# Optimization experiments

Measured on AMD Instinct MI355X. Metric: run time of the kernel, lower is better.

## Reference

```python
import jax, jax.numpy as jnp
import numpy as np

H = 32      # query heads
KV = 8      # kv heads
D = 128     # head_dim
HID = 4096
S = 4       # num sequences
L = 1024    # tokens per sequence
N = S * L   # total tokens
EPS = 1e-6
THETA = 10000.0
GROUPS = H // KV


def setup_inputs() -> dict:
    key = jax.random.key(0)
    ks = jax.random.split(key, 12)
    def w(k, shape, std):
        return jax.random.normal(k, shape, dtype=jnp.float32) * std
    return {
        "hidden": w(ks[0], (N, HID), 1.0),
        "mu_prev": w(ks[1], (N, HID), 1.0),
        "positions": jnp.tile(jnp.arange(L, dtype=jnp.int32), S),
        "Wq": w(ks[2], (H * D, HID), HID ** -0.5),
        "Wk": w(ks[3], (KV * D, HID), HID ** -0.5),
        "Wv": w(ks[4], (KV * D, HID), HID ** -0.5),
        "Wo": w(ks[5], (HID, H * D), (H * D) ** -0.5),
        "Wmq": w(ks[6], (H * D, HID), 0.01),
        "Wmk": w(ks[7], (KV * D, HID), 0.01),
        "Wmv": w(ks[8], (KV * D, HID), 0.01),
        "q_norm_w": jnp.ones((D,), jnp.float32),
        "k_norm_w": jnp.ones((D,), jnp.float32),
    }


def _rmsnorm(x, w):
    var = jnp.mean(jnp.square(x), axis=-1, keepdims=True)
    return x * jax.lax.rsqrt(var + EPS) * w


def _rope_cos_sin(positions):
    inv_freq = 1.0 / (THETA ** (jnp.arange(0, D, 2, dtype=jnp.float32) / D))  # [D/2]
    freqs = positions.astype(jnp.float32)[:, None] * inv_freq[None, :]        # [N, D/2]
    emb = jnp.concatenate([freqs, freqs], axis=-1)                            # [N, D]
    return jnp.cos(emb), jnp.sin(emb)


def _rotate_half(x):
    x1, x2 = jnp.split(x, 2, axis=-1)
    return jnp.concatenate([-x2, x1], axis=-1)


def _apply_rotary(x, cos, sin):
    # x: [N, h, D]; cos/sin: [N, D]
    return x * cos[:, None, :] + _rotate_half(x) * sin[:, None, :]


def reference(hidden, mu_prev, positions, Wq, Wk, Wv, Wo, Wmq, Wmk, Wmv, q_norm_w, k_norm_w):
    # QKV projections + mu-bias fusion
    q = hidden @ Wq.T + mu_prev @ Wmq.T     # [N, H*D]
    k = hidden @ Wk.T + mu_prev @ Wmk.T     # [N, KV*D]
    v = hidden @ Wv.T + mu_prev @ Wmv.T     # [N, KV*D]
    q = q.reshape(N, H, D)
    k = k.reshape(N, KV, D)
    v = v.reshape(N, KV, D)
    # QK RMSNorm
    q = _rmsnorm(q, q_norm_w)
    k = _rmsnorm(k, k_norm_w)
    # RoPE
    cos, sin = _rope_cos_sin(positions)
    q = _apply_rotary(q, cos, sin)
    k = _apply_rotary(k, cos, sin)
    # GQA: expand kv heads to match q heads
    k = jnp.repeat(k, GROUPS, axis=1)       # [N, H, D]
    v = jnp.repeat(v, GROUPS, axis=1)
    # Varlen causal attention: equal-length seqs -> batched [S, L, H, D]
    qs = q.reshape(S, L, H, D)
    ks = k.reshape(S, L, H, D)
    vs = v.reshape(S, L, H, D)
    scale = 1.0 / np.sqrt(D)
    scores = jnp.einsum("slhd,smhd->shlm", qs, ks) * scale   # [S, H, L, L]
    causal = jnp.tril(jnp.ones((L, L), dtype=bool))
    scores = jnp.where(causal, scores, jnp.finfo(scores.dtype).min)
    probs = jax.nn.softmax(scores, axis=-1)
    out = jnp.einsum("shlm,smhd->slhd", probs, vs)           # [S, L, H, D]
    out = out.reshape(N, H * D)
    return out @ Wo.T                                         # [N, HID]
```

## Files before the change

### kernel.cpp

```cpp
#include <hip/hip_runtime.h>
#include <hip/hip_bf16.h>
#include <stdint.h>

#define DEV static __device__ __forceinline__

typedef __bf16 bf16_t;
typedef __bf16 bf16x8 __attribute__((ext_vector_type(8)));
typedef __bf16 bf16x4 __attribute__((ext_vector_type(4)));
typedef float  f32x4  __attribute__((ext_vector_type(4)));


DEV void gload_lds16(const void* g, void* l) {
  __builtin_amdgcn_global_load_lds(
      (__attribute__((address_space(1))) void*)(uintptr_t)(g),
      (__attribute__((address_space(3))) void*)(uintptr_t)(l),
      16, 0, 0);
}

#define BARRIER() asm volatile("s_barrier" ::: "memory")
#define MFMA16(a, b, c) __builtin_amdgcn_mfma_f32_16x16x32_bf16((a), (b), (c), 0, 0, 0)

DEV void pack_pair_chunk(const float* __restrict__ A, const float* __restrict__ B,
                         bf16_t* __restrict__ dst, size_t i) {
  size_t r = i >> 10, c = i & 1023;
  float4 va = ((const float4*)A)[i];
  float4 vb = ((const float4*)B)[i];
  bf16x4 oa = {(bf16_t)va.x, (bf16_t)va.y, (bf16_t)va.z, (bf16_t)va.w};
  bf16x4 ob = {(bf16_t)vb.x, (bf16_t)vb.y, (bf16_t)vb.z, (bf16_t)vb.w};
  ((bf16x4*)dst)[r * 2048 + c] = oa;
  ((bf16x4*)dst)[r * 2048 + 1024 + c] = ob;
}

__global__ void k_pack_all(const float* __restrict__ hidden, const float* __restrict__ mu,
                           const float* __restrict__ Wq, const float* __restrict__ Wmq,
                           const float* __restrict__ Wk, const float* __restrict__ Wmk,
                           const float* __restrict__ Wv, const float* __restrict__ Wmv,
                           const float* __restrict__ Wo,
                           bf16_t* __restrict__ Xb, bf16_t* __restrict__ Wqkv,
                           bf16_t* __restrict__ Wob) {
  const size_t t0 = 4194304, t1 = 8388608, t2 = 9437184, t3 = 10485760, t4 = 14680064;
  size_t stride = (size_t)gridDim.x * blockDim.x;
  for (size_t i = (size_t)blockIdx.x * blockDim.x + threadIdx.x; i < t4; i += stride) {
    if (i < t0) {
      pack_pair_chunk(hidden, mu, Xb, i);
    } else if (i < t1) {
      pack_pair_chunk(Wq, Wmq, Wqkv, i - t0);
    } else if (i < t2) {
      pack_pair_chunk(Wk, Wmk, Wqkv + (size_t)4096 * 8192, i - t1);
    } else if (i < t3) {
      pack_pair_chunk(Wv, Wmv, Wqkv + (size_t)5120 * 8192, i - t2);
    } else {
      size_t j = i - t3;
      float4 v = ((const float4*)Wo)[j];
      bf16x4 o = {(bf16_t)v.x, (bf16_t)v.y, (bf16_t)v.z, (bf16_t)v.w};
      ((bf16x4*)Wob)[j] = o;
    }
  }
}

template<typename CT>
__global__ __launch_bounds__(256, 2) void k_gemm(
    const bf16_t* __restrict__ A, const bf16_t* __restrict__ B,
    CT* __restrict__ C, int M, int N, int Kfull) {
  __shared__ __align__(16) char lds[73728];
  const int tid = threadIdx.x, lane = tid & 63, wid = tid >> 6;
  const int l15 = lane & 15, lhi = lane >> 4;
  const int wm = wid >> 1, wn = wid & 1;
  const int bid = blockIdx.x, nwg = gridDim.x;
  const int cpx = nwg >> 3;
  const int swz = (bid & 7) * cpx + (bid >> 3);
  const int nbm = M >> 7;
  const int bm = swz % nbm, bn = swz / nbm;
  const int nkt = Kfull >> 5;

  const size_t rowK = (size_t)Kfull * 2;
  const int srow = tid >> 2;
  const int scs = (tid & 3) ^ (srow & 3);
  const char* sA = (const char*)A + ((size_t)bm * 128 + srow) * rowK + scs * 16;
  const char* sB = (const char*)B + ((size_t)bn * 256 + srow) * rowK + scs * 16;
  const size_t r64 = (size_t)64 * rowK;

  char* buf0 = lds;
  char* buf1 = lds + 24576;
  char* buf2 = lds + 49152;

#define STG(buf, kb) do { \
    gload_lds16(sA + (kb),            (buf) + tid * 16); \
    gload_lds16(sA + r64 + (kb),      (buf) + 4096 + tid * 16); \
    gload_lds16(sB + (kb),            (buf) + 8192 + tid * 16); \
    gload_lds16(sB + r64 + (kb),      (buf) + 12288 + tid * 16); \
    gload_lds16(sB + 2 * r64 + (kb),  (buf) + 16384 + tid * 16); \
    gload_lds16(sB + 3 * r64 + (kb),  (buf) + 20480 + tid * 16); } while (0)

  const int fch = (lhi ^ (l15 & 3)) << 4;
  int a_off[4], b_off[8];
#pragma unroll
  for (int mi = 0; mi < 4; ++mi) a_off[mi] = (wm * 64 + mi * 16 + l15) * 64 + fch;
#pragma unroll
  for (int ni = 0; ni < 8; ++ni) b_off[ni] = 8192 + (wn * 128 + ni * 16 + l15) * 64 + fch;

  f32x4 acc[4][8] = {};

  STG(buf0, 0);
  STG(buf1, 64);
  asm volatile("s_waitcnt vmcnt(6)" ::: "memory");
  BARRIER();

  char* cur = buf0;
  char* nxt = buf1;
  char* stg = buf2;
  for (int t = 0; t < nkt; ++t) {
    const int tn = (t + 2 < nkt) ? (t + 2) : (nkt - 1);
    STG(stg, (size_t)tn * 64);
    bf16x8 a[4], b[8];
#pragma unroll
    for (int mi = 0; mi < 4; ++mi) a[mi] = *(const bf16x8*)(cur + a_off[mi]);
#pragma unroll
    for (int ni = 0; ni < 8; ++ni) b[ni] = *(const bf16x8*)(cur + b_off[ni]);
    asm volatile("s_waitcnt lgkmcnt(0)" ::: "memory");
    __builtin_amdgcn_s_setprio(1);
#pragma unroll
    for (int mi = 0; mi < 4; ++mi)
#pragma unroll
      for (int ni = 0; ni < 8; ++ni)
        acc[mi][ni] = MFMA16(a[mi], b[ni], acc[mi][ni]);
    __builtin_amdgcn_s_setprio(0);
    asm volatile("s_waitcnt vmcnt(6)" ::: "memory");
    BARRIER();
    char* tmp = cur; cur = nxt; nxt = stg; stg = tmp;
  }

#pragma unroll
  for (int mi = 0; mi < 4; ++mi) {
    const int row0 = bm * 128 + wm * 64 + mi * 16 + 4 * lhi;
#pragma unroll
    for (int ni = 0; ni < 8; ++ni) {
      const int col = bn * 256 + wn * 128 + ni * 16 + l15;
#pragma unroll
      for (int i = 0; i < 4; ++i)
        C[(size_t)(row0 + i) * N + col] = (CT)acc[mi][ni][i];
    }
  }
#undef STG
}

__global__ __launch_bounds__(256) void k_norm_rope(
    const bf16_t* __restrict__ qkv, const int* __restrict__ pos,
    const float* __restrict__ qw, const float* __restrict__ kw,
    bf16_t* __restrict__ Q, bf16_t* __restrict__ Kk, bf16_t* __restrict__ V) {
  const int w = blockIdx.x * 4 + (threadIdx.x >> 6);
  const int lane = threadIdx.x & 63;
  const int n = w / 48, slot = w % 48;
  const bf16_t* row = qkv + (size_t)n * 6144;
  if (slot >= 40) {
    const int h2 = slot - 40;
    const int c = 5120 + h2 * 128 + lane;
    bf16_t* dst = V + ((size_t)n * 8 + h2) * 128;
    dst[lane] = row[c];
    dst[lane + 64] = row[c + 64];
    return;
  }
  const bool isq = slot < 32;
  const int h = isq ? slot : slot - 32;
  const int coff = (isq ? h * 128 : 4096 + h * 128) + lane;
  float x0 = (float)row[coff];
  float x1 = (float)row[coff + 64];
  float ss = x0 * x0 + x1 * x1;
#pragma unroll
  for (int m = 32; m; m >>= 1) ss += __shfl_xor(ss, m, 64);
  const float inv = rsqrtf(ss * (1.0f / 128.0f) + 1e-6f);
  const float* wgt = isq ? qw : kw;
  float y0 = x0 * inv * wgt[lane];
  float y1 = x1 * inv * wgt[lane + 64];
  const float ang = (float)pos[n] * expf((float)lane * -0.14391156608f);
  float sn, cs;
  sincosf(ang, &sn, &cs);
  float o0 = y0 * cs - y1 * sn;
  float o1 = y1 * cs + y0 * sn;
  bf16_t* dst = isq ? (Q + ((size_t)n * 32 + h) * 128) : (Kk + ((size_t)n * 8 + h) * 128);
  dst[lane] = (bf16_t)o0;
  dst[lane + 64] = (bf16_t)o1;
}

__global__ __launch_bounds__(256) void k_vt(const bf16_t* __restrict__ V,
                                            bf16_t* __restrict__ Vt) {
  __shared__ bf16_t T[64][136];
  const int blk = blockIdx.x;
  const int tt = blk & 15, kvh = (blk >> 4) & 7, s = blk >> 7;
  const int tok0 = tt * 64;
  const int tid = threadIdx.x;
#pragma unroll
  for (int k = 0; k < 4; ++k) {
    const int item = tid + k * 256;
    const int tok = item >> 4, d0 = (item & 15) * 8;
    bf16x8 v = *(const bf16x8*)(V + ((size_t)(s * 1024 + tok0 + tok) * 8 + kvh) * 128 + d0);
    *(bf16x8*)(&T[tok][d0]) = v;
  }
  __syncthreads();
#pragma unroll
  for (int k = 0; k < 4; ++k) {
    const int item = tid + k * 256;
    const int d = item & 127, oct = item >> 7;
    bf16x8 o;
#pragma unroll
    for (int j = 0; j < 8; ++j) o[j] = T[oct * 8 + j][d];
    *(bf16x8*)(Vt + ((size_t)((s * 8 + kvh) * 128 + d)) * 1024 + tok0 + oct * 8) = o;
  }
}

__global__ __launch_bounds__(256, 2) void k_attn(
    const bf16_t* __restrict__ Q, const bf16_t* __restrict__ Kk,
    const bf16_t* __restrict__ Vt, bf16_t* __restrict__ O) {
  __shared__ __align__(16) bf16_t Ks[2][64 * 128];
  __shared__ __align__(16) bf16_t Ps[4][32 * 72];
  const int b = blockIdx.x;
  const int x = b & 7, y = b >> 3;
  const int h = x * 4 + ((y >> 3) & 3);
  const int qb = 7 - (y & 7);
  const int s = y >> 5;
  const int kvh = h >> 2;
  const int tid = threadIdx.x, lane = tid & 63, wid = tid >> 6;
  const int l15 = lane & 15, lhi = lane >> 4;

  bf16x8 qf[2][4];
  {
    const int qrow = qb * 128 + wid * 32;
#pragma unroll
    for (int mt = 0; mt < 2; mt++) {
      const size_t base = ((size_t)(s * 1024 + qrow + mt * 16 + l15) * 32 + h) * 128;
#pragma unroll
      for (int kc = 0; kc < 4; kc++)
        qf[mt][kc] = *(const bf16x8*)(Q + base + kc * 32 + 8 * lhi);
    }
  }
  const bf16_t* Vtb = Vt + (size_t)((s * 8 + kvh) * 128) * 1024;

  f32x4 of[2][8] = {};
  float mx[2][4], li[2][4];
#pragma unroll
  for (int mt = 0; mt < 2; mt++)
#pragma unroll
    for (int i = 0; i < 4; i++) { mx[mt][i] = -1e30f; li[mt][i] = 0.f; }

  const int ktiles = (qb + 1) * 2;

  const int so = wid * 4096;
#define STAGE_K(kt_, buf_) do { _Pragma("unroll") \
    for (int c = 0; c < 4; ++c) { \
      const int o = so + c * 1024 + lane * 16; \
      const int krow = o >> 8; \
      const int cs = ((o >> 4) & 15) ^ (krow & 7); \
      const char* src = (const char*)(Kk + \
          ((size_t)(s * 1024 + (kt_) * 64 + krow) * 8 + kvh) * 128) + cs * 16; \
      gload_lds16(src, (char*)&Ks[buf_][0] + so + c * 1024); \
    } } while (0)

  STAGE_K(0, 0);
  asm volatile("s_waitcnt vmcnt(0)" ::: "memory");
  BARRIER();

  for (int kt = 0; kt < ktiles; kt++) {
    const int kv0 = kt * 64;
    const int buf = kt & 1;
    if (kt + 1 < ktiles) STAGE_K(kt + 1, buf ^ 1);

    f32x4 sf[2][4] = {};
#pragma unroll
    for (int kc = 0; kc < 4; kc++) {
      bf16x8 kf[4];
#pragma unroll
      for (int n = 0; n < 4; n++) {
        const int krow = n * 16 + l15;
        const int ci = (kc * 4 + lhi) ^ (krow & 7);
        kf[n] = *(const bf16x8*)(&Ks[buf][0] + krow * 128 + ci * 8);
      }
#pragma unroll
      for (int mt = 0; mt < 2; mt++)
#pragma unroll
        for (int n = 0; n < 4; n++)
          sf[mt][n] = MFMA16(qf[mt][kc], kf[n], sf[mt][n]);
    }

    const bool masked = (kt >= 2 * qb);
    const float scale = 0.08838834764831845f;
    float pv[2][4][4];
#pragma unroll
    for (int mt = 0; mt < 2; mt++) {
#pragma unroll
      for (int i = 0; i < 4; i++) {
        float rm = -1e30f;
#pragma unroll
        for (int n = 0; n < 4; n++) {
          float sv = sf[mt][n][i] * scale;
          if (masked) {
            const int kvg = kv0 + n * 16 + l15;
            const int qg = qb * 128 + wid * 32 + mt * 16 + 4 * lhi + i;
            if (kvg > qg) sv = -1e30f;
          }
          pv[mt][n][i] = sv;
          rm = fmaxf(rm, sv);
        }
#pragma unroll
        for (int mm = 1; mm < 16; mm <<= 1) rm = fmaxf(rm, __shfl_xor(rm, mm, 64));
        const float nm = fmaxf(mx[mt][i], rm);
        float ts = 0.f;
#pragma unroll
        for (int n = 0; n < 4; n++) {
          float e = __expf(pv[mt][n][i] - nm);
          pv[mt][n][i] = e;
          ts += e;
        }
#pragma unroll
        for (int mm = 1; mm < 16; mm <<= 1) ts += __shfl_xor(ts, mm, 64);
        const float al = __expf(mx[mt][i] - nm);
        li[mt][i] = li[mt][i] * al + ts;
        mx[mt][i] = nm;
#pragma unroll
        for (int n = 0; n < 8; n++) of[mt][n][i] *= al;
      }
    }

    bf16_t* myP = &Ps[wid][0];
#pragma unroll
    for (int mt = 0; mt < 2; mt++)
#pragma unroll
      for (int n = 0; n < 4; n++)
#pragma unroll
        for (int i = 0; i < 4; i++)
          myP[(mt * 16 + 4 * lhi + i) * 72 + n * 16 + l15] = (bf16_t)pv[mt][n][i];

#pragma unroll
    for (int kc = 0; kc < 2; kc++) {
      bf16x8 pf[2];
#pragma unroll
      for (int mt = 0; mt < 2; mt++)
        pf[mt] = *(const bf16x8*)(myP + (mt * 16 + l15) * 72 + kc * 32 + 8 * lhi);
#pragma unroll
      for (int n = 0; n < 8; n++) {
        const int d = n * 16 + l15;
        bf16x8 vf = *(const bf16x8*)(Vtb + (size_t)d * 1024 + kv0 + kc * 32 + 8 * lhi);
#pragma unroll
        for (int mt = 0; mt < 2; mt++)
          of[mt][n] = MFMA16(pf[mt], vf, of[mt][n]);
      }
    }

    if (kt + 1 < ktiles) {
      asm volatile("s_waitcnt vmcnt(0)" ::: "memory");
      BARRIER();
    }
  }
#undef STAGE_K

#pragma unroll
  for (int mt = 0; mt < 2; mt++) {
#pragma unroll
    for (int i = 0; i < 4; i++) {
      const float invl = 1.0f / li[mt][i];
      const int tokrow = qb * 128 + wid * 32 + mt * 16 + 4 * lhi + i;
      bf16_t* dst = O + (size_t)(s * 1024 + tokrow) * 4096 + h * 128;
#pragma unroll
      for (int n = 0; n < 8; n++)
        dst[n * 16 + l15] = (bf16_t)(of[mt][n][i] * invl);
    }
  }
}

extern "C" void kernel_launch(void* const* d_in, const int* in_sizes, int n_in,
                              void* d_out, int out_size, void* d_ws, size_t ws_size,
                              hipStream_t stream) {
  const float* hidden = (const float*)d_in[0];
  const float* mu     = (const float*)d_in[1];
  const int*   pos    = (const int*)d_in[2];
  const float* Wq  = (const float*)d_in[3];
  const float* Wk  = (const float*)d_in[4];
  const float* Wv  = (const float*)d_in[5];
  const float* Wo  = (const float*)d_in[6];
  const float* Wmq = (const float*)d_in[7];
  const float* Wmk = (const float*)d_in[8];
  const float* Wmv = (const float*)d_in[9];
  const float* qw  = (const float*)d_in[10];
  const float* kw  = (const float*)d_in[11];
  float* out = (float*)d_out;
  char* ws = (char*)d_ws;

  if (ws_size < 301989888u) return;

  bf16_t* Wqkv = (bf16_t*)(ws);
  bf16_t* Wob  = (bf16_t*)(ws + 100663296);
  bf16_t* Xb   = (bf16_t*)(ws + 134217728);
  bf16_t* Qb   = (bf16_t*)(ws + 134217728);
  bf16_t* Kb   = (bf16_t*)(ws + 167772160);
  bf16_t* Vb   = (bf16_t*)(ws + 176160768);
  bf16_t* VtG  = (bf16_t*)(ws + 184549376);
  bf16_t* qkv  = (bf16_t*)(ws + 201326592);
  bf16_t* Ob   = (bf16_t*)(ws + 201326592);

  k_pack_all<<<2048, 256, 0, stream>>>(hidden, mu, Wq, Wmq, Wk, Wmk, Wv, Wmv, Wo,
                                       Xb, Wqkv, Wob);
  k_gemm<bf16_t><<<768, 256, 0, stream>>>(Xb, Wqkv, qkv, 4096, 6144, 8192);
  k_norm_rope<<<49152, 256, 0, stream>>>(qkv, pos, qw, kw, Qb, Kb, Vb);
  k_vt<<<512, 256, 0, stream>>>(Vb, VtG);
  k_attn<<<1024, 256, 0, stream>>>(Qb, Kb, VtG, Ob);
  k_gemm<float><<<512, 256, 0, stream>>>(Ob, Wob, out, 4096, 4096, 4096);
}
```

Before: 880.1 us.

## Use 256x256 GEMM tiles with BK=64 and split-K for QKV projection

The GEMM kernel moves from 128x256 tiles with BK=32 and triple buffering to 256x256 tiles with BK=64 and double buffering, at one block per CU. This raises arithmetic intensity and cuts global and LDS traffic per FLOP. The QKV GEMM is split along K into two halves that write separate bf16 partial buffers, and the norm/RoPE kernel sums them while reading, so the grid stays full. The costs are extra partial-sum memory traffic, an extra bf16 rounding of the partials, and less latency hiding: only double buffering with a full vmcnt wait, at one block per CU.

```diff
diff --git a/kernel.cpp b/kernel.cpp
--- a/kernel.cpp
+++ b/kernel.cpp
@@ -58,113 +58,131 @@
   }
 }
 
-template<typename CT>
-__global__ __launch_bounds__(256, 2) void k_gemm(
+template<typename CT, int NSPLIT>
+__global__ __launch_bounds__(256, 1) void k_gemm256(
     const bf16_t* __restrict__ A, const bf16_t* __restrict__ B,
     CT* __restrict__ C, int M, int N, int Kfull) {
-  __shared__ __align__(16) char lds[73728];
-  const int tid = threadIdx.x, lane = tid & 63, wid = tid >> 6;
+  __shared__ __align__(16) char lds[131072];
+  const int tid = threadIdx.x, lane = tid & 63;
+  const int wid = tid >> 6;
   const int l15 = lane & 15, lhi = lane >> 4;
   const int wm = wid >> 1, wn = wid & 1;
   const int bid = blockIdx.x, nwg = gridDim.x;
   const int cpx = nwg >> 3;
   const int swz = (bid & 7) * cpx + (bid >> 3);
-  const int nbm = M >> 7;
-  const int bm = swz % nbm, bn = swz / nbm;
-  const int nkt = Kfull >> 5;
+  const int nbm = M >> 8;
+  const int tiles = nbm * (N >> 8);
+  const int ks = (NSPLIT > 1) ? (swz / tiles) : 0;
+  const int t0 = (NSPLIT > 1) ? (swz % tiles) : swz;
+  const int bm = t0 % nbm, bn = t0 / nbm;
+  const int Kloop = Kfull / NSPLIT;
+  const int nkt = Kloop >> 6;
 
   const size_t rowK = (size_t)Kfull * 2;
-  const int srow = tid >> 2;
-  const int scs = (tid & 3) ^ (srow & 3);
-  const char* sA = (const char*)A + ((size_t)bm * 128 + srow) * rowK + scs * 16;
-  const char* sB = (const char*)B + ((size_t)bn * 256 + srow) * rowK + scs * 16;
-  const size_t r64 = (size_t)64 * rowK;
-
-  char* buf0 = lds;
-  char* buf1 = lds + 24576;
-  char* buf2 = lds + 49152;
-
-#define STG(buf, kb) do { \
-    gload_lds16(sA + (kb),            (buf) + tid * 16); \
-    gload_lds16(sA + r64 + (kb),      (buf) + 4096 + tid * 16); \
-    gload_lds16(sB + (kb),            (buf) + 8192 + tid * 16); \
-    gload_lds16(sB + r64 + (kb),      (buf) + 12288 + tid * 16); \
-    gload_lds16(sB + 2 * r64 + (kb),  (buf) + 16384 + tid * 16); \
-    gload_lds16(sB + 3 * r64 + (kb),  (buf) + 20480 + tid * 16); } while (0)
-
-  const int fch = (lhi ^ (l15 & 3)) << 4;
-  int a_off[4], b_off[8];
-#pragma unroll
-  for (int mi = 0; mi < 4; ++mi) a_off[mi] = (wm * 64 + mi * 16 + l15) * 64 + fch;
-#pragma unroll
-  for (int ni = 0; ni < 8; ++ni) b_off[ni] = 8192 + (wn * 128 + ni * 16 + l15) * 64 + fch;
-
-  f32x4 acc[4][8] = {};
-
-  STG(buf0, 0);
-  STG(buf1, 64);
-  asm volatile("s_waitcnt vmcnt(6)" ::: "memory");
+  const size_t kbase = (size_t)ks * Kloop * 2;
+  const int srow = tid >> 3;
+  const int scs = (tid & 7) ^ (srow & 7);
+  const char* sA = (const char*)A + ((size_t)bm * 256 + srow) * rowK + kbase + scs * 16;
+  const char* sB = (const char*)B + ((size_t)bn * 256 + srow) * rowK + kbase + scs * 16;
+  const size_t r32 = (size_t)32 * rowK;
+
+#define STG(bufo, kb) do { _Pragma("unroll") \
+    for (int j = 0; j < 8; ++j) { \
+      gload_lds16(sA + (size_t)j * r32 + (kb), lds + (bufo) + j * 4096 + tid * 16); \
+      gload_lds16(sB + (size_t)j * r32 + (kb), lds + (bufo) + 32768 + j * 4096 + tid * 16); \
+    } } while (0)
+
+  const int coff0 = ((lhi ^ (l15 & 7)) << 4);
+  const int coff1 = (((4 + lhi) ^ (l15 & 7)) << 4);
+  int aRow[8], bRow[8];
+#pragma unroll
+  for (int mi = 0; mi < 8; ++mi) aRow[mi] = (wm * 128 + mi * 16 + l15) << 7;
+#pragma unroll
+  for (int ni = 0; ni < 8; ++ni) bRow[ni] = 32768 + ((wn * 128 + ni * 16 + l15) << 7);
+
+  f32x4 acc[8][8] = {};
+
+  STG(0, 0);
+  asm volatile("s_waitcnt vmcnt(0)" ::: "memory");
   BARRIER();
 
-  char* cur = buf0;
-  char* nxt = buf1;
-  char* stg = buf2;
+  int bufo = 0;
   for (int t = 0; t < nkt; ++t) {
-    const int tn = (t + 2 < nkt) ? (t + 2) : (nkt - 1);
-    STG(stg, (size_t)tn * 64);
-    bf16x8 a[4], b[8];
-#pragma unroll
-    for (int mi = 0; mi < 4; ++mi) a[mi] = *(const bf16x8*)(cur + a_off[mi]);
-#pragma unroll
-    for (int ni = 0; ni < 8; ++ni) b[ni] = *(const bf16x8*)(cur + b_off[ni]);
+    if (t + 1 < nkt) STG(bufo ^ 65536, (size_t)(t + 1) * 128);
+    bf16x8 a[8][2], b[8][2];
+#pragma unroll
+    for (int mi = 0; mi < 8; ++mi)
+      a[mi][0] = *(const bf16x8*)(lds + bufo + aRow[mi] + coff0);
+#pragma unroll
+    for (int ni = 0; ni < 8; ++ni)
+      b[ni][0] = *(const bf16x8*)(lds + bufo + bRow[ni] + coff0);
+#pragma unroll
+    for (int mi = 0; mi < 8; ++mi)
+      a[mi][1] = *(const bf16x8*)(lds + bufo + aRow[mi] + coff1);
+#pragma unroll
+    for (int ni = 0; ni < 8; ++ni)
+      b[ni][1] = *(const bf16x8*)(lds + bufo + bRow[ni] + coff1);
+    asm volatile("s_waitcnt lgkmcnt(15)" ::: "memory");
+    __builtin_amdgcn_s_setprio(1);
+#pragma unroll
+    for (int mi = 0; mi < 8; ++mi)
+#pragma unroll
+      for (int ni = 0; ni < 8; ++ni)
+        acc[mi][ni] = MFMA16(a[mi][0], b[ni][0], acc[mi][ni]);
+    __builtin_amdgcn_s_setprio(0);
     asm volatile("s_waitcnt lgkmcnt(0)" ::: "memory");
     __builtin_amdgcn_s_setprio(1);
 #pragma unroll
-    for (int mi = 0; mi < 4; ++mi)
+    for (int mi = 0; mi < 8; ++mi)
 #pragma unroll
       for (int ni = 0; ni < 8; ++ni)
-        acc[mi][ni] = MFMA16(a[mi], b[ni], acc[mi][ni]);
+        acc[mi][ni] = MFMA16(a[mi][1], b[ni][1], acc[mi][ni]);
     __builtin_amdgcn_s_setprio(0);
-    asm volatile("s_waitcnt vmcnt(6)" ::: "memory");
+    asm volatile("s_waitcnt vmcnt(0)" ::: "memory");
     BARRIER();
-    char* tmp = cur; cur = nxt; nxt = stg; stg = tmp;
-  }
-
-#pragma unroll
-  for (int mi = 0; mi < 4; ++mi) {
-    const int row0 = bm * 128 + wm * 64 + mi * 16 + 4 * lhi;
+    bufo ^= 65536;
+  }
+
+  CT* Cp = C + (size_t)ks * M * N;
+#pragma unroll
+  for (int mi = 0; mi < 8; ++mi) {
+    const int row0 = bm * 256 + wm * 128 + mi * 16 + 4 * lhi;
 #pragma unroll
     for (int ni = 0; ni < 8; ++ni) {
       const int col = bn * 256 + wn * 128 + ni * 16 + l15;
 #pragma unroll
       for (int i = 0; i < 4; ++i)
-        C[(size_t)(row0 + i) * N + col] = (CT)acc[mi][ni][i];
+        Cp[(size_t)(row0 + i) * N + col] = (CT)acc[mi][ni][i];
     }
   }
 #undef STG
 }
 
 __global__ __launch_bounds__(256) void k_norm_rope(
-    const bf16_t* __restrict__ qkv, const int* __restrict__ pos,
+    const bf16_t* __restrict__ qkvA, const bf16_t* __restrict__ qkvB,
+    const int* __restrict__ pos,
     const float* __restrict__ qw, const float* __restrict__ kw,
     bf16_t* __restrict__ Q, bf16_t* __restrict__ Kk, bf16_t* __restrict__ V) {
   const int w = blockIdx.x * 4 + (threadIdx.x >> 6);
   const int lane = threadIdx.x & 63;
   const int n = w / 48, slot = w % 48;
-  const bf16_t* row = qkv + (size_t)n * 6144;
+  const bf16_t* rowA = qkvA + (size_t)n * 6144;
+  const bf16_t* rowB = qkvB + (size_t)n * 6144;
   if (slot >= 40) {
     const int h2 = slot - 40;
     const int c = 5120 + h2 * 128 + lane;
+    float x0 = (float)rowA[c] + (float)rowB[c];
+    float x1 = (float)rowA[c + 64] + (float)rowB[c + 64];
     bf16_t* dst = V + ((size_t)n * 8 + h2) * 128;
-    dst[lane] = row[c];
-    dst[lane + 64] = row[c + 64];
+    dst[lane] = (bf16_t)x0;
+    dst[lane + 64] = (bf16_t)x1;
     return;
   }
   const bool isq = slot < 32;
   const int h = isq ? slot : slot - 32;
   const int coff = (isq ? h * 128 : 4096 + h * 128) + lane;
-  float x0 = (float)row[coff];
-  float x1 = (float)row[coff + 64];
+  float x0 = (float)rowA[coff] + (float)rowB[coff];
+  float x1 = (float)rowA[coff + 64] + (float)rowB[coff + 64];
   float ss = x0 * x0 + x1 * x1;
 #pragma unroll
   for (int m = 32; m; m >>= 1) ss += __shfl_xor(ss, m, 64);
@@ -393,14 +411,15 @@
   bf16_t* Kb   = (bf16_t*)(ws + 167772160);
   bf16_t* Vb   = (bf16_t*)(ws + 176160768);
   bf16_t* VtG  = (bf16_t*)(ws + 184549376);
-  bf16_t* qkv  = (bf16_t*)(ws + 201326592);
+  bf16_t* qkvA = (bf16_t*)(ws + 201326592);
+  bf16_t* qkvB = (bf16_t*)(ws + 251658240);
   bf16_t* Ob   = (bf16_t*)(ws + 201326592);
 
   k_pack_all<<<2048, 256, 0, stream>>>(hidden, mu, Wq, Wmq, Wk, Wmk, Wv, Wmv, Wo,
                                        Xb, Wqkv, Wob);
-  k_gemm<bf16_t><<<768, 256, 0, stream>>>(Xb, Wqkv, qkv, 4096, 6144, 8192);
-  k_norm_rope<<<49152, 256, 0, stream>>>(qkv, pos, qw, kw, Qb, Kb, Vb);
+  k_gemm256<bf16_t, 2><<<768, 256, 0, stream>>>(Xb, Wqkv, qkvA, 4096, 6144, 8192);
+  k_norm_rope<<<49152, 256, 0, stream>>>(qkvA, qkvB, pos, qw, kw, Qb, Kb, Vb);
   k_vt<<<512, 256, 0, stream>>>(Vb, VtG);
   k_attn<<<1024, 256, 0, stream>>>(Qb, Kb, VtG, Ob);
-  k_gemm<float><<<512, 256, 0, stream>>>(Ob, Wob, out, 4096, 4096, 4096);
-}
+  k_gemm256<float, 1><<<256, 256, 0, stream>>>(Ob, Wob, out, 4096, 4096, 4096);
+}
```

After: 859.4 us. -2.4%, faster.
